# Kernel tuning notes

Measured on AMD Instinct MI355X. Metric: run time of the kernel, lower is better.

Reference implementation:

```python
import jax, jax.numpy as jnp
import numpy as np

B, H, D, DV, N, M = 1, 8, 64, 64, 2048, 128


def setup_inputs() -> dict:
    key = jax.random.key(0)
    k1, k2, k3, k4 = jax.random.split(key, 4)
    keys = jax.random.normal(k1, (B, H, D, N), dtype=jnp.float32)
    values = jax.random.normal(k2, (B, H, DV, N), dtype=jnp.float32)
    queries = jax.random.normal(k3, (B, H, D, N), dtype=jnp.float32)
    # orthonormal random features: QR of (m, key_dim) gaussian (reduced QR, m >= key_dim)
    raw = np.asarray(jax.random.normal(k4, (M, D), dtype=jnp.float32), dtype=np.float64)
    features = jnp.asarray(np.linalg.qr(raw)[0], dtype=jnp.float32)  # (M, D)
    return {"keys": keys, "values": values, "queries": queries, "features": features}


def reference(keys, values, queries, features):
    b, h, d, n = keys.shape
    dv = values.shape[2]
    m = features.shape[0]
    phi_scale = 1.0 / jnp.sqrt(jnp.asarray(m, keys.dtype))
    # flatten heads into batch, move locations to axis 1: (B*H, N, D)
    k = keys.reshape(b * h, d, n).transpose(0, 2, 1)
    v = values.reshape(b * h, dv, n).transpose(0, 2, 1)
    q = queries.reshape(b * h, d, n).transpose(0, 2, 1)

    def phi(x):  # (BH, N, D) -> (BH, N, M); f=[relu], h(x)=1.0
        return jax.nn.relu(jnp.einsum('bnd,md->bnm', x, features)) * phi_scale

    phi_k = phi(k)
    phi_q = phi(q)
    # causal linear attention: prefix sums of phi_k (x) v outer products
    kv = jnp.cumsum(phi_k[:, :, :, None] * v[:, :, None, :], axis=1)  # (BH, N, M, DV)
    out = jnp.einsum('bnm,bnmv->bnv', phi_q, kv)                      # (BH, N, DV)
    norm = jnp.einsum('bnm,bnm->bn', phi_q, jnp.cumsum(phi_k, axis=1))
    out = out / norm[:, :, None]
    out = out.transpose(0, 2, 1).reshape(b, h, dv, n)
    return out
```

## Files before the change

kernel.cpp:

```cpp
#include <hip/hip_runtime.h>


#define BH 8
#define D 64
#define DV 64
#define NSEQ 2048
#define M 128
#define CHK 64
#define NC (NSEQ / CHK)
#define PHI_SCALE 0.08838834764831845f

typedef unsigned int uint;
typedef unsigned short ushort;
typedef __attribute__((ext_vector_type(8))) short bf16x8;
typedef __attribute__((ext_vector_type(4))) short bf16x4;
typedef __attribute__((ext_vector_type(4))) float f32x4;
#define MFMA16(a, b, c) __builtin_amdgcn_mfma_f32_16x16x32_bf16((a), (b), (c), 0, 0, 0)

__device__ __forceinline__ short f2bf(float x) {
    uint u = __float_as_uint(x);
    u += 0x7fffu + ((u >> 16) & 1u);
    return (short)(u >> 16);
}
__device__ __forceinline__ float bf2f(short b) {
    return __uint_as_float(((uint)(ushort)b) << 16);
}

#define SWZ64(r, c)  ((r) * 64  + ((c) ^ (((r) & 7) << 3)))
#define SWZ128(r, c) ((r) * 128 + ((c) ^ (((r) & 7) << 3)))

__global__ __launch_bounds__(256) void favor_p1(
    const float* __restrict__ keys, const float* __restrict__ values,
    const float* __restrict__ queries, const float* __restrict__ features,
    ushort* __restrict__ St, float* __restrict__ z,
    ushort* __restrict__ pQg, ushort* __restrict__ pKg)
{
    const int bh = blockIdx.x >> 5, c = blockIdx.x & 31, n0 = c * CHK;
    const int tid = threadIdx.x;
    const int lane = tid & 63, wid = tid >> 6, quad = lane >> 4, l16 = lane & 15;

    __shared__ ulong2 smv[4096];
    short* sF    = (short*)smv;
    short* sPKmn = (short*)smv + 8192;
    short* sPQt  = (short*)smv + 16384;
    short* sPKt  = (short*)smv + 24576;

    const float* Kb = keys    + bh * D * NSEQ + n0 + 16 * wid + l16;
    const float* Qb = queries + bh * D * NSEQ + n0 + 16 * wid + l16;
    bf16x8 bK[2], aQ[2], aV[2];
    for (int h = 0; h < 2; ++h)
        for (int j = 0; j < 8; ++j) {
            const int d = 32 * h + 8 * quad + j;
            bK[h][j] = f2bf(Kb[d * NSEQ]);
            aQ[h][j] = f2bf(Qb[d * NSEQ]);
        }
    {
        const float* Vb = values + bh * DV * NSEQ + n0;
        for (int h = 0; h < 2; ++h) {
            const float4* vp = (const float4*)(Vb + (16 * wid + l16) * NSEQ + 32 * h + 8 * quad);
            float4 v0 = vp[0], v1 = vp[1];
            aV[h][0] = f2bf(v0.x); aV[h][1] = f2bf(v0.y);
            aV[h][2] = f2bf(v0.z); aV[h][3] = f2bf(v0.w);
            aV[h][4] = f2bf(v1.x); aV[h][5] = f2bf(v1.y);
            aV[h][6] = f2bf(v1.z); aV[h][7] = f2bf(v1.w);
        }
    }
    for (int k = 0; k < 8; ++k) {
        const int i = tid + 256 * k;
        float4 f = ((const float4*)features)[i];
        const int e = 4 * i, row = e >> 6, col = e & 63;
        bf16x4 bq;
        bq[0] = f2bf(f.x); bq[1] = f2bf(f.y); bq[2] = f2bf(f.z); bq[3] = f2bf(f.w);
        *(bf16x4*)(sF + SWZ64(row, col)) = bq;
    }
    __syncthreads();

    for (int mt = 0; mt < 8; ++mt) {
        f32x4 aMN = {0.f,0.f,0.f,0.f}, aQm = {0.f,0.f,0.f,0.f}, aKm = {0.f,0.f,0.f,0.f};
        for (int h = 0; h < 2; ++h) {
            bf16x8 fF = *(const bf16x8*)(sF + SWZ64(16 * mt + l16, 32 * h + 8 * quad));
            aMN = MFMA16(fF, bK[h], aMN);
            aQm = MFMA16(aQ[h], fF, aQm);
            aKm = MFMA16(bK[h], fF, aKm);
        }
        for (int r = 0; r < 4; ++r) {
            const int mr = 16 * mt + 4 * quad + r;
            sPKmn[SWZ64(mr, 16 * wid + l16)] = f2bf(fmaxf(aMN[r], 0.f) * PHI_SCALE);
            const int nr = 16 * wid + 4 * quad + r;
            sPQt[SWZ128(nr, 16 * mt + l16)] = f2bf(fmaxf(aQm[r], 0.f) * PHI_SCALE);
            sPKt[SWZ128(nr, 16 * mt + l16)] = f2bf(fmaxf(aKm[r], 0.f) * PHI_SCALE);
        }
    }
    __syncthreads();

    if (tid < 128) {
        float s = 0.f;
        for (int k = 0; k < 8; ++k) {
            bf16x8 v8 = *(const bf16x8*)(sPKmn + SWZ64(tid, 8 * k));
            for (int j = 0; j < 8; ++j) s += bf2f(v8[j]);
        }
        z[(bh * NC + c) * M + tid] = s;
    }

    {
        ushort* So = St + (size_t)(bh * NC + c) * (DV * M);
        for (int mt = 0; mt < 8; ++mt) {
            f32x4 acc = {0.f,0.f,0.f,0.f};
            for (int h = 0; h < 2; ++h) {
                bf16x8 bP = *(const bf16x8*)(sPKmn + SWZ64(16 * mt + l16, 32 * h + 8 * quad));
                acc = MFMA16(aV[h], bP, acc);
            }
            for (int r = 0; r < 4; ++r)
                So[(16 * wid + 4 * quad + r) * M + 16 * mt + l16] = (ushort)f2bf(acc[r]);
        }
    }

    {
        ushort* pQc = pQg + (size_t)(bh * NC + c) * 8192;
        ushort* pKc = pKg + (size_t)(bh * NC + c) * 8192;
        const ulong2* sq = (const ulong2*)sPQt;
        const ulong2* sk = (const ulong2*)sPKt;
        for (int i = tid; i < 1024; i += 256) {
            ((ulong2*)pQc)[i] = sq[i];
            ((ulong2*)pKc)[i] = sk[i];
        }
    }
}

__global__ __launch_bounds__(256) void favor_p2(ushort* __restrict__ St,
                                                float* __restrict__ z)
{
    const int gid = blockIdx.x * 256 + threadIdx.x;
    if (blockIdx.x < 256) {
        const int bh = gid >> 13, vm = gid & 8191;
        ushort* p = St + (size_t)bh * NC * 8192 + vm;
        float vals[NC];
        #pragma unroll
        for (int cc = 0; cc < NC; ++cc) vals[cc] = bf2f(p[cc * 8192]);
        float run = 0.f;
        #pragma unroll
        for (int cc = 0; cc < NC; ++cc) { p[cc * 8192] = (ushort)f2bf(run); run += vals[cc]; }
    } else {
        const int i = gid - 65536;
        if (i < BH * M) {
            const int bh = i >> 7, m = i & 127;
            float* p = z + bh * NC * M + m;
            float vals[NC];
            #pragma unroll
            for (int cc = 0; cc < NC; ++cc) vals[cc] = p[cc * M];
            float run = 0.f;
            #pragma unroll
            for (int cc = 0; cc < NC; ++cc) { p[cc * M] = run; run += vals[cc]; }
        }
    }
}

__global__ __launch_bounds__(256) void favor_p3(
    const float* __restrict__ values, const ushort* __restrict__ St,
    const float* __restrict__ z, const ushort* __restrict__ pQg,
    const ushort* __restrict__ pKg, float* __restrict__ out)
{
    const int bh = blockIdx.x >> 5, c = blockIdx.x & 31, n0 = c * CHK;
    const int tid = threadIdx.x;
    const int lane = tid & 63, wid = tid >> 6, quad = lane >> 4, l16 = lane & 15;

    __shared__ ulong2 smv[3184];
    short* sPQt = (short*)smv;
    short* sPKt = (short*)smv + 8192;
    short* sV   = (short*)smv + 16384;
    short* sAm  = (short*)smv + 20480;
    float* sNm  = (float*)((char*)smv + 49152);
    float* sNmP = (float*)((char*)smv + 49408);
    float* sZ   = (float*)((char*)smv + 50432);
    float* sOut = (float*)smv;

    {
        const ulong2* pQc = (const ulong2*)(pQg + (size_t)(bh * NC + c) * 8192);
        const ulong2* pKc = (const ulong2*)(pKg + (size_t)(bh * NC + c) * 8192);
        ulong2* dq = (ulong2*)sPQt;
        ulong2* dk = (ulong2*)sPKt;
        for (int i = tid; i < 1024; i += 256) {
            dq[i] = pQc[i];
            dk[i] = pKc[i];
        }
    }
    {
        const int v = tid >> 2, cb = (tid & 3) * 16;
        const float4* vp = (const float4*)(values + (bh * DV + v) * NSEQ + n0 + cb);
        float4 f0 = vp[0], f1 = vp[1], f2 = vp[2], f3 = vp[3];
        bf16x8 lo, hi;
        lo[0] = f2bf(f0.x); lo[1] = f2bf(f0.y); lo[2] = f2bf(f0.z); lo[3] = f2bf(f0.w);
        lo[4] = f2bf(f1.x); lo[5] = f2bf(f1.y); lo[6] = f2bf(f1.z); lo[7] = f2bf(f1.w);
        hi[0] = f2bf(f2.x); hi[1] = f2bf(f2.y); hi[2] = f2bf(f2.z); hi[3] = f2bf(f2.w);
        hi[4] = f2bf(f3.x); hi[5] = f2bf(f3.y); hi[6] = f2bf(f3.z); hi[7] = f2bf(f3.w);
        *(bf16x8*)(sV + SWZ64(v, cb))     = lo;
        *(bf16x8*)(sV + SWZ64(v, cb + 8)) = hi;
    }
    if (tid < 128) sZ[tid] = z[(bh * NC + c) * M + tid];
    __syncthreads();

    f32x4 accO[4], accC[4];
    for (int t = 0; t < 4; ++t) { accO[t] = (f32x4){0.f,0.f,0.f,0.f}; accC[t] = (f32x4){0.f,0.f,0.f,0.f}; }
    for (int mt = 0; mt < 4; ++mt) {
        bf16x8 aP = *(const bf16x8*)(sPQt + SWZ128(16 * wid + l16, 32 * mt + 8 * quad));
        for (int jt = 0; jt < 4; ++jt) {
            bf16x8 bK2 = *(const bf16x8*)(sPKt + SWZ128(16 * jt + l16, 32 * mt + 8 * quad));
            accC[jt] = MFMA16(aP, bK2, accC[jt]);
        }
    }
    float rsum[4] = {0.f, 0.f, 0.f, 0.f};
    for (int jt = 0; jt < 4; ++jt)
        for (int r = 0; r < 4; ++r) {
            const int n = 16 * wid + 4 * quad + r;
            const int j = 16 * jt + l16;
            const float av = (j <= n) ? accC[jt][r] : 0.f;
            rsum[r] += av;
            sAm[SWZ64(n, j)] = f2bf(av);
        }
    for (int r = 0; r < 4; ++r) {
        float s = rsum[r];
        s += __shfl_xor(s, 1); s += __shfl_xor(s, 2);
        s += __shfl_xor(s, 4); s += __shfl_xor(s, 8);
        if (l16 == 0) sNm[16 * wid + 4 * quad + r] = s;
    }

    {
        const ushort* Sb = St + (size_t)(bh * NC + c) * (DV * M);
        for (int mt = 0; mt < 4; ++mt) {
            bf16x8 aP = *(const bf16x8*)(sPQt + SWZ128(16 * wid + l16, 32 * mt + 8 * quad));
            for (int vt = 0; vt < 4; ++vt) {
                bf16x8 bS = *(const bf16x8*)(Sb + (16 * vt + l16) * M + 32 * mt + 8 * quad);
                accO[vt] = MFMA16(aP, bS, accO[vt]);
            }
        }
    }
    {
        const int n = tid & 63, g = tid >> 6;
        float s = 0.f;
        for (int mm = 0; mm < 32; ++mm) {
            const int m = 32 * g + ((mm + n) & 31);
            s += bf2f(sPQt[SWZ128(n, m)]) * sZ[m];
        }
        sNmP[n * 4 + g] = s;
    }
    __syncthreads();

    for (int jh = 0; jh < 2; ++jh) {
        bf16x8 aA = *(const bf16x8*)(sAm + SWZ64(16 * wid + l16, 32 * jh + 8 * quad));
        for (int vt = 0; vt < 4; ++vt) {
            bf16x8 bV = *(const bf16x8*)(sV + SWZ64(16 * vt + l16, 32 * jh + 8 * quad));
            accO[vt] = MFMA16(aA, bV, accO[vt]);
        }
    }
    if (tid < 64)
        sNm[tid] += sNmP[tid * 4] + sNmP[tid * 4 + 1] + sNmP[tid * 4 + 2] + sNmP[tid * 4 + 3];
    __syncthreads();

    for (int vt = 0; vt < 4; ++vt)
        for (int r = 0; r < 4; ++r) {
            const int n = 16 * wid + 4 * quad + r, v = 16 * vt + l16;
            sOut[n * 65 + v] = accO[vt][r] / sNm[n];
        }
    __syncthreads();
    for (int i = tid; i < 4096; i += 256) {
        const int v = i >> 6, n = i & 63;
        out[(bh * DV + v) * NSEQ + n0 + n] = sOut[n * 65 + v];
    }
}

extern "C" void kernel_launch(void* const* d_in, const int* in_sizes, int n_in,
                              void* d_out, int out_size, void* d_ws, size_t ws_size,
                              hipStream_t stream)
{
    (void)in_sizes; (void)n_in; (void)out_size; (void)ws_size;
    const float* keys     = (const float*)d_in[0];
    const float* values   = (const float*)d_in[1];
    const float* queries  = (const float*)d_in[2];
    const float* features = (const float*)d_in[3];
    float* outp = (float*)d_out;

    char* w = (char*)d_ws;
    ushort* St  = (ushort*)w;
    float*  z   = (float*)(w + (size_t)4 * 1024 * 1024);
    ushort* pQg = (ushort*)(w + (size_t)4 * 1024 * 1024 + 128 * 1024);
    ushort* pKg = (ushort*)(w + (size_t)8 * 1024 * 1024 + 128 * 1024);

    favor_p1<<<dim3(BH * NC), dim3(256), 0, stream>>>(keys, values, queries, features,
                                                      St, z, pQg, pKg);
    favor_p2<<<dim3(260), dim3(256), 0, stream>>>(St, z);
    favor_p3<<<dim3(BH * NC), dim3(256), 0, stream>>>(values, St, z, pQg, pKg, outp);
}
```

Before: 89.25 us.

## Split feature and value dimensions across blocks to double grid parallelism

Phase 1 now splits the 128 random features into two halves per chunk, and phase 3 splits the 64 value columns into two halves, doubling each grid to 512 blocks with less shared memory per block. Phase 2 splits each column's chunk prefix scan into two halves joined through a shared-memory carry, and phase 3 prefetches the prefix-state tiles into registers early. The goal is better occupancy and latency hiding on a GPU with many compute units, since 256 blocks underfill it. In exchange, phase 1 recomputes the K and Q loads and conversions in both halves, and phase 3 duplicates the phi_Q·phi_K score matrix and normaliser work.

After: 88.49 us. No clear change (-0.9%).

```diff
diff --git a/kernel.cpp b/kernel.cpp
--- a/kernel.cpp
+++ b/kernel.cpp
@@ -29,22 +29,31 @@
 #define SWZ64(r, c)  ((r) * 64  + ((c) ^ (((r) & 7) << 3)))
 #define SWZ128(r, c) ((r) * 128 + ((c) ^ (((r) & 7) << 3)))
 
-__global__ __launch_bounds__(256) void favor_p1(
+__global__ __launch_bounds__(256, 2) void favor_p1(
     const float* __restrict__ keys, const float* __restrict__ values,
     const float* __restrict__ queries, const float* __restrict__ features,
     ushort* __restrict__ St, float* __restrict__ z,
     ushort* __restrict__ pQg, ushort* __restrict__ pKg)
 {
-    const int bh = blockIdx.x >> 5, c = blockIdx.x & 31, n0 = c * CHK;
+    const int mh = blockIdx.x >> 8, cid = blockIdx.x & 255;
+    const int bh = cid >> 5, c = cid & 31, n0 = c * CHK;
     const int tid = threadIdx.x;
     const int lane = tid & 63, wid = tid >> 6, quad = lane >> 4, l16 = lane & 15;
 
-    __shared__ ulong2 smv[4096];
+    __shared__ ulong2 smv[2048];
     short* sF    = (short*)smv;
-    short* sPKmn = (short*)smv + 8192;
-    short* sPQt  = (short*)smv + 16384;
-    short* sPKt  = (short*)smv + 24576;
-
+    short* sPKmn = (short*)smv + 4096;
+    short* sPQt  = (short*)smv + 8192;
+    short* sPKt  = (short*)smv + 12288;
+
+    for (int k = 0; k < 4; ++k) {
+        const int i = tid + 256 * k;
+        float4 f = ((const float4*)features)[mh * 1024 + i];
+        const int e = 4 * i, row = e >> 6, col = e & 63;
+        bf16x4 bq;
+        bq[0] = f2bf(f.x); bq[1] = f2bf(f.y); bq[2] = f2bf(f.z); bq[3] = f2bf(f.w);
+        *(bf16x4*)(sF + SWZ64(row, col)) = bq;
+    }
     const float* Kb = keys    + bh * D * NSEQ + n0 + 16 * wid + l16;
     const float* Qb = queries + bh * D * NSEQ + n0 + 16 * wid + l16;
     bf16x8 bK[2], aQ[2], aV[2];
@@ -65,17 +74,9 @@
             aV[h][6] = f2bf(v1.z); aV[h][7] = f2bf(v1.w);
         }
     }
-    for (int k = 0; k < 8; ++k) {
-        const int i = tid + 256 * k;
-        float4 f = ((const float4*)features)[i];
-        const int e = 4 * i, row = e >> 6, col = e & 63;
-        bf16x4 bq;
-        bq[0] = f2bf(f.x); bq[1] = f2bf(f.y); bq[2] = f2bf(f.z); bq[3] = f2bf(f.w);
-        *(bf16x4*)(sF + SWZ64(row, col)) = bq;
-    }
-    __syncthreads();
-
-    for (int mt = 0; mt < 8; ++mt) {
+    __syncthreads();
+
+    for (int mt = 0; mt < 4; ++mt) {
         f32x4 aMN = {0.f,0.f,0.f,0.f}, aQm = {0.f,0.f,0.f,0.f}, aKm = {0.f,0.f,0.f,0.f};
         for (int h = 0; h < 2; ++h) {
             bf16x8 fF = *(const bf16x8*)(sF + SWZ64(16 * mt + l16, 32 * h + 8 * quad));
@@ -87,31 +88,29 @@
             const int mr = 16 * mt + 4 * quad + r;
             sPKmn[SWZ64(mr, 16 * wid + l16)] = f2bf(fmaxf(aMN[r], 0.f) * PHI_SCALE);
             const int nr = 16 * wid + 4 * quad + r;
-            sPQt[SWZ128(nr, 16 * mt + l16)] = f2bf(fmaxf(aQm[r], 0.f) * PHI_SCALE);
-            sPKt[SWZ128(nr, 16 * mt + l16)] = f2bf(fmaxf(aKm[r], 0.f) * PHI_SCALE);
-        }
-    }
-    __syncthreads();
-
-    if (tid < 128) {
+            sPQt[SWZ64(nr, 16 * mt + l16)] = f2bf(fmaxf(aQm[r], 0.f) * PHI_SCALE);
+            sPKt[SWZ64(nr, 16 * mt + l16)] = f2bf(fmaxf(aKm[r], 0.f) * PHI_SCALE);
+        }
+    }
+    __syncthreads();
+
+    if (tid < 64) {
         float s = 0.f;
-        for (int k = 0; k < 8; ++k) {
-            bf16x8 v8 = *(const bf16x8*)(sPKmn + SWZ64(tid, 8 * k));
-            for (int j = 0; j < 8; ++j) s += bf2f(v8[j]);
-        }
-        z[(bh * NC + c) * M + tid] = s;
+        for (int n = 0; n < 64; ++n) s += bf2f(sPKmn[SWZ64(tid, (n + tid) & 63)]);
+        z[(bh * NC + c) * M + mh * 64 + tid] = s;
     }
 
     {
         ushort* So = St + (size_t)(bh * NC + c) * (DV * M);
-        for (int mt = 0; mt < 8; ++mt) {
+        for (int mt = 0; mt < 4; ++mt) {
             f32x4 acc = {0.f,0.f,0.f,0.f};
             for (int h = 0; h < 2; ++h) {
                 bf16x8 bP = *(const bf16x8*)(sPKmn + SWZ64(16 * mt + l16, 32 * h + 8 * quad));
                 acc = MFMA16(aV[h], bP, acc);
             }
             for (int r = 0; r < 4; ++r)
-                So[(16 * wid + 4 * quad + r) * M + 16 * mt + l16] = (ushort)f2bf(acc[r]);
+                So[(16 * wid + 4 * quad + r) * M + mh * 64 + 16 * mt + l16] =
+                    (ushort)f2bf(acc[r]);
         }
     }
 
@@ -120,59 +119,81 @@
         ushort* pKc = pKg + (size_t)(bh * NC + c) * 8192;
         const ulong2* sq = (const ulong2*)sPQt;
         const ulong2* sk = (const ulong2*)sPKt;
-        for (int i = tid; i < 1024; i += 256) {
-            ((ulong2*)pQc)[i] = sq[i];
-            ((ulong2*)pKc)[i] = sk[i];
-        }
-    }
-}
-
-__global__ __launch_bounds__(256) void favor_p2(ushort* __restrict__ St,
-                                                float* __restrict__ z)
+        for (int i = tid; i < 512; i += 256) {
+            const int row = i >> 3, q = i & 7;
+            ((ulong2*)pQc)[row * 16 + mh * 8 + q] = sq[i];
+            ((ulong2*)pKc)[row * 16 + mh * 8 + q] = sk[i];
+        }
+    }
+}
+
+__global__ __launch_bounds__(256, 2) void favor_p2(ushort* __restrict__ St,
+                                                   float* __restrict__ z)
 {
-    const int gid = blockIdx.x * 256 + threadIdx.x;
-    if (blockIdx.x < 256) {
-        const int bh = gid >> 13, vm = gid & 8191;
+    __shared__ float carry[128];
+    const int tid = threadIdx.x;
+    if (blockIdx.x < 512) {
+        const int col = blockIdx.x * 128 + (tid & 127);
+        const int half = tid >> 7;
+        const int bh = col >> 13, vm = col & 8191;
         ushort* p = St + (size_t)bh * NC * 8192 + vm;
+        float vals[16];
+        #pragma unroll
+        for (int k = 0; k < 16; ++k) vals[k] = bf2f(p[(16 * half + k) * 8192]);
+        if (half == 0) {
+            float total = 0.f;
+            #pragma unroll
+            for (int k = 0; k < 16; ++k) total += vals[k];
+            carry[tid] = total;
+        }
+        __syncthreads();
+        float run = (half == 0) ? 0.f : carry[tid & 127];
+        #pragma unroll
+        for (int k = 0; k < 16; ++k) {
+            p[(16 * half + k) * 8192] = (ushort)f2bf(run);
+            run += vals[k];
+        }
+    } else {
+        const int i = (blockIdx.x - 512) * 256 + tid;
+        const int bh = i >> 7, m = i & 127;
+        float* p = z + bh * NC * M + m;
         float vals[NC];
         #pragma unroll
-        for (int cc = 0; cc < NC; ++cc) vals[cc] = bf2f(p[cc * 8192]);
+        for (int cc = 0; cc < NC; ++cc) vals[cc] = p[cc * M];
         float run = 0.f;
         #pragma unroll
-        for (int cc = 0; cc < NC; ++cc) { p[cc * 8192] = (ushort)f2bf(run); run += vals[cc]; }
-    } else {
-        const int i = gid - 65536;
-        if (i < BH * M) {
-            const int bh = i >> 7, m = i & 127;
-            float* p = z + bh * NC * M + m;
-            float vals[NC];
-            #pragma unroll
-            for (int cc = 0; cc < NC; ++cc) vals[cc] = p[cc * M];
-            float run = 0.f;
-            #pragma unroll
-            for (int cc = 0; cc < NC; ++cc) { p[cc * M] = run; run += vals[cc]; }
-        }
-    }
-}
-
-__global__ __launch_bounds__(256) void favor_p3(
+        for (int cc = 0; cc < NC; ++cc) { p[cc * M] = run; run += vals[cc]; }
+    }
+}
+
+__global__ __launch_bounds__(256, 2) void favor_p3(
     const float* __restrict__ values, const ushort* __restrict__ St,
     const float* __restrict__ z, const ushort* __restrict__ pQg,
     const ushort* __restrict__ pKg, float* __restrict__ out)
 {
-    const int bh = blockIdx.x >> 5, c = blockIdx.x & 31, n0 = c * CHK;
+    const int vh = blockIdx.x >> 8, cid = blockIdx.x & 255;
+    const int bh = cid >> 5, c = cid & 31, n0 = c * CHK;
     const int tid = threadIdx.x;
     const int lane = tid & 63, wid = tid >> 6, quad = lane >> 4, l16 = lane & 15;
 
-    __shared__ ulong2 smv[3184];
+    __shared__ ulong2 smv[2928];
     short* sPQt = (short*)smv;
     short* sPKt = (short*)smv + 8192;
     short* sV   = (short*)smv + 16384;
-    short* sAm  = (short*)smv + 20480;
-    float* sNm  = (float*)((char*)smv + 49152);
-    float* sNmP = (float*)((char*)smv + 49408);
-    float* sZ   = (float*)((char*)smv + 50432);
+    short* sAm  = (short*)smv + 18432;
+    float* sNm  = (float*)((char*)smv + 45056);
+    float* sNmP = (float*)((char*)smv + 45312);
+    float* sZ   = (float*)((char*)smv + 46336);
     float* sOut = (float*)smv;
+
+    const ushort* Sb = St + (size_t)(bh * NC + c) * (DV * M);
+    bf16x8 bS[4][2];
+    #pragma unroll
+    for (int mt = 0; mt < 4; ++mt)
+        #pragma unroll
+        for (int vt = 0; vt < 2; ++vt)
+            bS[mt][vt] = *(const bf16x8*)(Sb + (vh * 32 + 16 * vt + l16) * M
+                                             + 32 * mt + 8 * quad);
 
     {
         const ulong2* pQc = (const ulong2*)(pQg + (size_t)(bh * NC + c) * 8192);
@@ -185,22 +206,21 @@
         }
     }
     {
-        const int v = tid >> 2, cb = (tid & 3) * 16;
-        const float4* vp = (const float4*)(values + (bh * DV + v) * NSEQ + n0 + cb);
-        float4 f0 = vp[0], f1 = vp[1], f2 = vp[2], f3 = vp[3];
-        bf16x8 lo, hi;
-        lo[0] = f2bf(f0.x); lo[1] = f2bf(f0.y); lo[2] = f2bf(f0.z); lo[3] = f2bf(f0.w);
-        lo[4] = f2bf(f1.x); lo[5] = f2bf(f1.y); lo[6] = f2bf(f1.z); lo[7] = f2bf(f1.w);
-        hi[0] = f2bf(f2.x); hi[1] = f2bf(f2.y); hi[2] = f2bf(f2.z); hi[3] = f2bf(f2.w);
-        hi[4] = f2bf(f3.x); hi[5] = f2bf(f3.y); hi[6] = f2bf(f3.z); hi[7] = f2bf(f3.w);
-        *(bf16x8*)(sV + SWZ64(v, cb))     = lo;
-        *(bf16x8*)(sV + SWZ64(v, cb + 8)) = hi;
+        const int vrow = tid >> 3, cb = (tid & 7) * 8;
+        const float4* vp = (const float4*)(values + (bh * DV + vh * 32 + vrow) * NSEQ
+                                                  + n0 + cb);
+        float4 f0 = vp[0], f1 = vp[1];
+        bf16x8 w;
+        w[0] = f2bf(f0.x); w[1] = f2bf(f0.y); w[2] = f2bf(f0.z); w[3] = f2bf(f0.w);
+        w[4] = f2bf(f1.x); w[5] = f2bf(f1.y); w[6] = f2bf(f1.z); w[7] = f2bf(f1.w);
+        *(bf16x8*)(sV + SWZ64(vrow, cb)) = w;
     }
     if (tid < 128) sZ[tid] = z[(bh * NC + c) * M + tid];
     __syncthreads();
 
-    f32x4 accO[4], accC[4];
-    for (int t = 0; t < 4; ++t) { accO[t] = (f32x4){0.f,0.f,0.f,0.f}; accC[t] = (f32x4){0.f,0.f,0.f,0.f}; }
+    f32x4 accO[2], accC[4];
+    accO[0] = (f32x4){0.f,0.f,0.f,0.f}; accO[1] = (f32x4){0.f,0.f,0.f,0.f};
+    for (int t = 0; t < 4; ++t) accC[t] = (f32x4){0.f,0.f,0.f,0.f};
     for (int mt = 0; mt < 4; ++mt) {
         bf16x8 aP = *(const bf16x8*)(sPQt + SWZ128(16 * wid + l16, 32 * mt + 8 * quad));
         for (int jt = 0; jt < 4; ++jt) {
@@ -224,15 +244,10 @@
         if (l16 == 0) sNm[16 * wid + 4 * quad + r] = s;
     }
 
-    {
-        const ushort* Sb = St + (size_t)(bh * NC + c) * (DV * M);
-        for (int mt = 0; mt < 4; ++mt) {
-            bf16x8 aP = *(const bf16x8*)(sPQt + SWZ128(16 * wid + l16, 32 * mt + 8 * quad));
-            for (int vt = 0; vt < 4; ++vt) {
-                bf16x8 bS = *(const bf16x8*)(Sb + (16 * vt + l16) * M + 32 * mt + 8 * quad);
-                accO[vt] = MFMA16(aP, bS, accO[vt]);
-            }
-        }
+    for (int mt = 0; mt < 4; ++mt) {
+        bf16x8 aP = *(const bf16x8*)(sPQt + SWZ128(16 * wid + l16, 32 * mt + 8 * quad));
+        for (int vt = 0; vt < 2; ++vt)
+            accO[vt] = MFMA16(aP, bS[mt][vt], accO[vt]);
     }
     {
         const int n = tid & 63, g = tid >> 6;
@@ -247,7 +262,7 @@
 
     for (int jh = 0; jh < 2; ++jh) {
         bf16x8 aA = *(const bf16x8*)(sAm + SWZ64(16 * wid + l16, 32 * jh + 8 * quad));
-        for (int vt = 0; vt < 4; ++vt) {
+        for (int vt = 0; vt < 2; ++vt) {
             bf16x8 bV = *(const bf16x8*)(sV + SWZ64(16 * vt + l16, 32 * jh + 8 * quad));
             accO[vt] = MFMA16(aA, bV, accO[vt]);
         }
@@ -256,15 +271,15 @@
         sNm[tid] += sNmP[tid * 4] + sNmP[tid * 4 + 1] + sNmP[tid * 4 + 2] + sNmP[tid * 4 + 3];
     __syncthreads();
 
-    for (int vt = 0; vt < 4; ++vt)
+    for (int vt = 0; vt < 2; ++vt)
         for (int r = 0; r < 4; ++r) {
-            const int n = 16 * wid + 4 * quad + r, v = 16 * vt + l16;
-            sOut[n * 65 + v] = accO[vt][r] / sNm[n];
-        }
-    __syncthreads();
-    for (int i = tid; i < 4096; i += 256) {
-        const int v = i >> 6, n = i & 63;
-        out[(bh * DV + v) * NSEQ + n0 + n] = sOut[n * 65 + v];
+            const int n = 16 * wid + 4 * quad + r, vl = 16 * vt + l16;
+            sOut[n * 33 + vl] = accO[vt][r] / sNm[n];
+        }
+    __syncthreads();
+    for (int i = tid; i < 2048; i += 256) {
+        const int vl = i >> 6, n = i & 63;
+        out[(bh * DV + vh * 32 + vl) * NSEQ + n0 + n] = sOut[n * 33 + vl];
     }
 }
 
@@ -285,8 +300,8 @@
     ushort* pQg = (ushort*)(w + (size_t)4 * 1024 * 1024 + 128 * 1024);
     ushort* pKg = (ushort*)(w + (size_t)8 * 1024 * 1024 + 128 * 1024);
 
-    favor_p1<<<dim3(BH * NC), dim3(256), 0, stream>>>(keys, values, queries, features,
-                                                      St, z, pQg, pKg);
-    favor_p2<<<dim3(260), dim3(256), 0, stream>>>(St, z);
-    favor_p3<<<dim3(BH * NC), dim3(256), 0, stream>>>(values, St, z, pQg, pKg, outp);
-}
+    favor_p1<<<dim3(512), dim3(256), 0, stream>>>(keys, values, queries, features,
+                                                  St, z, pQg, pKg);
+    favor_p2<<<dim3(516), dim3(256), 0, stream>>>(St, z);
+    favor_p3<<<dim3(512), dim3(256), 0, stream>>>(values, St, z, pQg, pKg, outp);
+}
```
